# Kernel optimization log

Measured on AMD Instinct MI355X. Metric: run time of the kernel, lower is better.

## Reference

```python
import jax, jax.numpy as jnp
import numpy as np

B, C, W, H = 4, 256, 64, 64

def setup_inputs() -> dict:
    key = jax.random.key(0)
    ks = jax.random.split(key, 6)
    return {
        "fm_source": jax.random.normal(ks[0], (B, C, W, H), dtype=jnp.float32),
        "fm_reference": jax.random.normal(ks[1], (B, C, W, H), dtype=jnp.float32),
        "w_lambda": jax.random.normal(ks[2], (1, C, 1, 1), dtype=jnp.float32) * 0.05,
        "b_lambda": jax.random.normal(ks[3], (1,), dtype=jnp.float32) * 0.05,
        "w_beta": jax.random.normal(ks[4], (1, C, 1, 1), dtype=jnp.float32) * 0.05,
        "b_beta": jax.random.normal(ks[5], (1,), dtype=jnp.float32) * 0.05,
    }

def reference(fm_source, fm_reference, w_lambda, b_lambda, w_beta, b_beta):
    b, c, w, h = fm_reference.shape
    n = w * h
    # 1x1 convs on the reference feature map -> per-pixel scalars, flattened to [B, N]
    wl = w_lambda.reshape(c)
    wb = w_beta.reshape(c)
    ref_flat = fm_reference.reshape(b, c, n)   # [B, C, N]
    src_flat = fm_source.reshape(b, c, n)      # [B, C, N]
    old_lambda = jnp.einsum("bcn,c->bn", ref_flat, wl) + b_lambda[0]  # [B, N]
    old_beta = jnp.einsum("bcn,c->bn", ref_flat, wb) + b_beta[0]      # [B, N]
    # energy[b, i, j] = <src pixel i, ref pixel j> over channels
    energy = jnp.einsum("bci,bcj->bij", src_flat, ref_flat)  # [B, N, N]
    attention = jax.nn.softmax(energy, axis=-1)              # softmax over ref pixels j
    # new_lambda[b, i] = sum_j old_lambda[b, j] * attention[b, i, j]
    new_lambda = jnp.einsum("bj,bij->bi", old_lambda, attention).reshape(b, 1, w, h)
    new_beta = jnp.einsum("bj,bij->bi", old_beta, attention).reshape(b, 1, w, h)
    # broadcast modulation over the 256 channels
    return new_lambda * fm_source + new_beta
```

## Files before the change

kernel.cpp:

```cpp
#include <hip/hip_runtime.h>


#define B_ 4
#define C_ 256
#define N_ 4096
#define LOG2E 1.44269504f
#define SHIFT2 86.5617f
#define JSLICE 16
#define BN_ (B_ * N_)

typedef _Float16 half_t;
typedef _Float16 v8h  __attribute__((ext_vector_type(8)));
typedef float    v16f __attribute__((ext_vector_type(16)));

__global__ void k_transpose(const float* __restrict__ src,
                            const float* __restrict__ ref,
                            half_t* __restrict__ s16, half_t* __restrict__ r16) {
    __shared__ float tile[64][65];
    int z  = blockIdx.z;
    int b  = z & 3;
    const float* in  = (z < B_) ? src : ref;
    half_t*      out = (z < B_) ? s16 : r16;
    float scale      = (z < B_) ? LOG2E : 1.0f;
    int c0 = blockIdx.y * 64;
    int n0 = blockIdx.x * 64;
    int tx = threadIdx.x & 15, ty = threadIdx.x >> 4;
#pragma unroll
    for (int q = 0; q < 4; q++) {
        int c = ty + q * 16;
        float4 v = *(const float4*)(in + ((size_t)b * C_ + c0 + c) * N_ + n0 + tx * 4);
        tile[c][tx * 4 + 0] = v.x;
        tile[c][tx * 4 + 1] = v.y;
        tile[c][tx * 4 + 2] = v.z;
        tile[c][tx * 4 + 3] = v.w;
    }
    __syncthreads();
    int r   = threadIdx.x & 31;
    int lhi = (threadIdx.x >> 5) & 1;
    int wv  = threadIdx.x >> 6;
#pragma unroll
    for (int nt = 0; nt < 2; nt++) {
        int nl = nt * 32 + r;
        v8h o;
#pragma unroll
        for (int e = 0; e < 8; e++)
            o[e] = (half_t)(tile[wv * 16 + lhi * 8 + e][nl] * scale);
        size_t tj = (size_t)(n0 >> 5) + nt;
        size_t kb = (size_t)(c0 >> 4) + wv;
        *(v8h*)(out + ((((size_t)b * 128 + tj) * 16 + kb) * 64 + (threadIdx.x & 63)) * 8) = o;
    }
}

__global__ void k_oldlb(const float* __restrict__ ref,
                        const float* __restrict__ wl, const float* __restrict__ bl,
                        const float* __restrict__ wb, const float* __restrict__ bb,
                        float* __restrict__ oldL, float* __restrict__ oldB) {
    int b = blockIdx.y;
    int n = blockIdx.x * 64 + threadIdx.x;
    const float* p = ref + (size_t)b * C_ * N_ + n;
    float aL = bl[0], aB = bb[0];
#pragma unroll 8
    for (int c = 0; c < C_; c++) {
        float v = p[(size_t)c * N_];
        aL += v * wl[c];
        aB += v * wb[c];
    }
    oldL[(size_t)b * N_ + n] = aL;
    oldB[(size_t)b * N_ + n] = aB;
}

__global__ __launch_bounds__(256, 3) void k_flash(
        const half_t* __restrict__ sT, const half_t* __restrict__ rT,
        const float* __restrict__ oldL, const float* __restrict__ oldB,
        float* __restrict__ part ) {
    int bid    = blockIdx.x;
    int b      = bid & 3;
    int jslice = (bid >> 2) & (JSLICE - 1);
    int itile  = bid >> 6;
    int wv     = threadIdx.x >> 6;
    int lane   = threadIdx.x & 63;
    int l31    = lane & 31, lhi = lane >> 5;
    int ti     = itile * 4 + wv;
    int i0     = ti * 32;
    int j0     = jslice * (N_ / JSLICE);
    int tj0    = j0 >> 5;

    const half_t* aP = sT + (((size_t)b * 128 + ti) * 16) * 512 + (size_t)lane * 8;
    v8h a[16];
#pragma unroll
    for (int kb = 0; kb < 16; kb++) a[kb] = *(const v8h*)(aP + (size_t)kb * 512);

    const half_t* bP  = rT + (((size_t)b * 128 + tj0) * 16) * 512 + (size_t)lane * 8;
    const float*  oLp = oldL + (size_t)b * N_ + j0 + l31;
    const float*  oBp = oldB + (size_t)b * N_ + j0 + l31;

    float sp[16], sl[16], sb[16];
#pragma unroll
    for (int r = 0; r < 16; r++) { sp[r] = 0.f; sl[r] = 0.f; sb[r] = 0.f; }

    const int NT = (N_ / JSLICE) / 32;
    for (int jt = 0; jt < NT; jt++) {
        const half_t* bt = bP + (size_t)jt * 8192;
        v16f acc;
#pragma unroll
        for (int r = 0; r < 16; r++) acc[r] = -SHIFT2;
#pragma unroll
        for (int kb = 0; kb < 16; kb++) {
            v8h bf = *(const v8h*)(bt + (size_t)kb * 512);
            acc = __builtin_amdgcn_mfma_f32_32x32x16_f16(a[kb], bf, acc, 0, 0, 0);
        }
        float lam = oLp[jt * 32], bet = oBp[jt * 32];
#pragma unroll
        for (int r = 0; r < 16; r++) {
            float p = __builtin_amdgcn_exp2f(acc[r]);
            sp[r] += p;
            sl[r] += p * lam;
            sb[r] += p * bet;
        }
    }

    float* pSP = part + ((size_t)jslice * 3 + 0) * BN_;
    float* pSL = part + ((size_t)jslice * 3 + 1) * BN_;
    float* pSB = part + ((size_t)jslice * 3 + 2) * BN_;
#pragma unroll
    for (int r = 0; r < 16; r++) {
        float tp = sp[r], tl = sl[r], tb = sb[r];
#pragma unroll
        for (int m = 1; m <= 16; m <<= 1) {
            tp += __shfl_xor(tp, m, 64);
            tl += __shfl_xor(tl, m, 64);
            tb += __shfl_xor(tb, m, 64);
        }
        if (l31 == 0) {
            int row = (r & 3) + 8 * (r >> 2) + 4 * lhi;
            size_t ig = (size_t)b * N_ + i0 + row;
            pSP[ig] = tp; pSL[ig] = tl; pSB[ig] = tb;
        }
    }
}

__global__ void k_reduce(const float* __restrict__ part,
                         float* __restrict__ newL, float* __restrict__ newB) {
    int bn = blockIdx.x * 256 + threadIdx.x;
    float sp = 0.f, sl = 0.f, sb = 0.f;
#pragma unroll
    for (int s = 0; s < JSLICE; s++) {
        sp += part[((size_t)s * 3 + 0) * BN_ + bn];
        sl += part[((size_t)s * 3 + 1) * BN_ + bn];
        sb += part[((size_t)s * 3 + 2) * BN_ + bn];
    }
    float inv = 1.0f / sp;
    newL[bn] = sl * inv;
    newB[bn] = sb * inv;
}

__global__ void k_modulate(const float* __restrict__ src,
                           const float* __restrict__ newL,
                           const float* __restrict__ newB,
                           float* __restrict__ out) {
    size_t idx = ((size_t)blockIdx.x * 256 + threadIdx.x) * 4;
    int b = (int)(idx >> 20);
    int n = (int)(idx & (size_t)(N_ - 1));
    size_t bn = (size_t)b * N_ + n;
    float4 L = *(const float4*)(newL + bn);
    float4 T = *(const float4*)(newB + bn);
    float4 s = *(const float4*)(src + idx);
    float4 o;
    o.x = L.x * s.x + T.x;
    o.y = L.y * s.y + T.y;
    o.z = L.z * s.z + T.z;
    o.w = L.w * s.w + T.w;
    *(float4*)(out + idx) = o;
}

extern "C" void kernel_launch(void* const* d_in, const int* in_sizes, int n_in,
                              void* d_out, int out_size, void* d_ws, size_t ws_size,
                              hipStream_t stream) {
    const float* src = (const float*)d_in[0];
    const float* ref = (const float*)d_in[1];
    const float* wl  = (const float*)d_in[2];
    const float* bl  = (const float*)d_in[3];
    const float* wb  = (const float*)d_in[4];
    const float* bb  = (const float*)d_in[5];
    float* out = (float*)d_out;

    float* oldL = (float*)d_ws;
    float* oldB = oldL + BN_;
    float* newL = oldB + BN_;
    float* newB = newL + BN_;
    float* part = newB + BN_;
    size_t needF  = ((size_t)4 + 3 * JSLICE) * BN_ * sizeof(float);
    size_t need16 = (size_t)2 * B_ * N_ * C_ * sizeof(half_t);
    half_t* s16;
    if (ws_size >= needF + need16) s16 = (half_t*)((char*)d_ws + needF);
    else                           s16 = (half_t*)d_out;
    half_t* r16 = s16 + (size_t)B_ * N_ * C_;

    k_transpose<<<dim3(N_ / 64, C_ / 64, 2 * B_), 256, 0, stream>>>(src, ref, s16, r16);
    k_oldlb<<<dim3(N_ / 64, B_), 64, 0, stream>>>(ref, wl, bl, wb, bb, oldL, oldB);
    k_flash<<<2048, 256, 0, stream>>>(s16, r16, oldL, oldB, part);
    k_reduce<<<BN_ / 256, 256, 0, stream>>>(part, newL, newB);
    k_modulate<<<(B_ * C_ * N_) / (256 * 4), 256, 0, stream>>>(src, newL, newB, out);
}
```

Before: 171.4 us.

## Stage reference tiles through double-buffered LDS in flash kernel; split oldlb channel reduction

The flash kernel now loads each 32-column reference tile cooperatively into a double-buffered shared-memory array, prefetching the next tile into registers while the MFMAs and exp work on the current one. Before, each of the four waves loaded the same B fragments from global memory. This cuts redundant global/L2 traffic and hides load latency, at the cost of 32KB of LDS per block and a barrier every iteration, which may limit occupancy at 3 blocks per CU. The oldlb kernel also splits the channel sum across four waves with a shared-memory reduction, to raise parallelism in a small kernel.

```diff
diff --git a/kernel.cpp b/kernel.cpp
--- a/kernel.cpp
+++ b/kernel.cpp
@@ -8,6 +8,7 @@
 #define SHIFT2 86.5617f
 #define JSLICE 16
 #define BN_ (B_ * N_)
+#define NT_ 8
 
 typedef _Float16 half_t;
 typedef _Float16 v8h  __attribute__((ext_vector_type(8)));
@@ -55,30 +56,45 @@
                         const float* __restrict__ wl, const float* __restrict__ bl,
                         const float* __restrict__ wb, const float* __restrict__ bb,
                         float* __restrict__ oldL, float* __restrict__ oldB) {
-    int b = blockIdx.y;
-    int n = blockIdx.x * 64 + threadIdx.x;
-    const float* p = ref + (size_t)b * C_ * N_ + n;
-    float aL = bl[0], aB = bb[0];
+    int b  = blockIdx.y;
+    int n0 = blockIdx.x * 64;
+    int nl = threadIdx.x & 63;
+    int cq = threadIdx.x >> 6;
+    const float* p = ref + ((size_t)b * C_ + cq * 64) * N_ + n0 + nl;
+    float aL = 0.f, aB = 0.f;
 #pragma unroll 8
-    for (int c = 0; c < C_; c++) {
+    for (int c = 0; c < 64; c++) {
         float v = p[(size_t)c * N_];
-        aL += v * wl[c];
-        aB += v * wb[c];
-    }
-    oldL[(size_t)b * N_ + n] = aL;
-    oldB[(size_t)b * N_ + n] = aB;
+        aL += v * wl[cq * 64 + c];
+        aB += v * wb[cq * 64 + c];
+    }
+    __shared__ float red[8][64];
+    red[cq][nl]     = aL;
+    red[4 + cq][nl] = aB;
+    __syncthreads();
+    if (threadIdx.x < 64) {
+        int t = threadIdx.x;
+        oldL[(size_t)b * N_ + n0 + t] =
+            red[0][t] + red[1][t] + red[2][t] + red[3][t] + bl[0];
+    } else if (threadIdx.x < 128) {
+        int t = threadIdx.x - 64;
+        oldB[(size_t)b * N_ + n0 + t] =
+            red[4][t] + red[5][t] + red[6][t] + red[7][t] + bb[0];
+    }
 }
 
 __global__ __launch_bounds__(256, 3) void k_flash(
         const half_t* __restrict__ sT, const half_t* __restrict__ rT,
         const float* __restrict__ oldL, const float* __restrict__ oldB,
         float* __restrict__ part ) {
+    __shared__ half_t lds[2][8192];
     int bid    = blockIdx.x;
     int b      = bid & 3;
     int jslice = (bid >> 2) & (JSLICE - 1);
     int itile  = bid >> 6;
-    int wv     = threadIdx.x >> 6;
-    int lane   = threadIdx.x & 63;
+    int tid    = threadIdx.x;
+    int wv     = tid >> 6;
+    int lane   = tid & 63;
     int l31    = lane & 31, lhi = lane >> 5;
     int ti     = itile * 4 + wv;
     int i0     = ti * 32;
@@ -90,7 +106,7 @@
 #pragma unroll
     for (int kb = 0; kb < 16; kb++) a[kb] = *(const v8h*)(aP + (size_t)kb * 512);
 
-    const half_t* bP  = rT + (((size_t)b * 128 + tj0) * 16) * 512 + (size_t)lane * 8;
+    const half_t* bBase = rT + (((size_t)b * 128 + tj0) * 16) * 512;
     const float*  oLp = oldL + (size_t)b * N_ + j0 + l31;
     const float*  oBp = oldB + (size_t)b * N_ + j0 + l31;
 
@@ -98,9 +114,21 @@
 #pragma unroll
     for (int r = 0; r < 16; r++) { sp[r] = 0.f; sl[r] = 0.f; sb[r] = 0.f; }
 
-    const int NT = (N_ / JSLICE) / 32;
-    for (int jt = 0; jt < NT; jt++) {
-        const half_t* bt = bP + (size_t)jt * 8192;
+    v8h st[4];
+    {
+        const v8h* g = (const v8h*)bBase;
+        st[0] = g[tid]; st[1] = g[tid + 256]; st[2] = g[tid + 512]; st[3] = g[tid + 768];
+        v8h* l = (v8h*)lds[0];
+        l[tid] = st[0]; l[tid + 256] = st[1]; l[tid + 512] = st[2]; l[tid + 768] = st[3];
+    }
+
+    for (int jt = 0; jt < NT_; jt++) {
+        __syncthreads();
+        if (jt + 1 < NT_) {
+            const v8h* g = (const v8h*)(bBase + (size_t)(jt + 1) * 8192);
+            st[0] = g[tid]; st[1] = g[tid + 256]; st[2] = g[tid + 512]; st[3] = g[tid + 768];
+        }
+        const half_t* bt = lds[jt & 1] + (size_t)lane * 8;
         v16f acc;
 #pragma unroll
         for (int r = 0; r < 16; r++) acc[r] = -SHIFT2;
@@ -116,6 +144,10 @@
             sp[r] += p;
             sl[r] += p * lam;
             sb[r] += p * bet;
+        }
+        if (jt + 1 < NT_) {
+            v8h* l = (v8h*)lds[(jt + 1) & 1];
+            l[tid] = st[0]; l[tid + 256] = st[1]; l[tid + 512] = st[2]; l[tid + 768] = st[3];
         }
     }
 
@@ -197,7 +229,7 @@
     half_t* r16 = s16 + (size_t)B_ * N_ * C_;
 
     k_transpose<<<dim3(N_ / 64, C_ / 64, 2 * B_), 256, 0, stream>>>(src, ref, s16, r16);
-    k_oldlb<<<dim3(N_ / 64, B_), 64, 0, stream>>>(ref, wl, bl, wb, bb, oldL, oldB);
+    k_oldlb<<<dim3(N_ / 64, B_), 256, 0, stream>>>(ref, wl, bl, wb, bb, oldL, oldB);
     k_flash<<<2048, 256, 0, stream>>>(s16, r16, oldL, oldB, part);
     k_reduce<<<BN_ / 256, 256, 0, stream>>>(part, newL, newB);
     k_modulate<<<(B_ * C_ * N_) / (256 * 4), 256, 0, stream>>>(src, newL, newB, out);
```

Result: slower. 219.4 us (+28.0%).
